# Performance work log

Measured on AMD Instinct MI355X. Metric: run time of the kernel, lower is better.

## Reference

```python
import jax, jax.numpy as jnp
import numpy as np

B, H, W, C = 64, 224, 224, 3
P = 16
DIM = 768
DEPTH = 12
NH, DH = 12, 64
FF = 3072
NPATCH = (H // P) * (W // P)   # 196
L = NPATCH + 1                 # 197 tokens (CLS + patches)
KEEP = int(L * (1.0 - 0.75))   # 49 unmasked tokens


def setup_inputs() -> dict:
    key = jax.random.key(0)
    ks = jax.random.split(key, 16)
    s = 0.02
    inp = {
        'inputs': jax.random.normal(ks[0], (B, H, W, C), jnp.float32),
        'conv_w': jax.random.normal(ks[1], (P, P, C, DIM), jnp.float32) * s,
        'ct':     jax.random.normal(ks[2], (1, 1, DIM), jnp.float32) * s,
        'pe':     jax.random.normal(ks[3], (1, L, DIM), jnp.float32) * s,
        'ln1_s': jnp.ones((DEPTH, DIM), jnp.float32),
        'ln1_b': jnp.zeros((DEPTH, DIM), jnp.float32),
        'qkv_w': jax.random.normal(ks[4], (DEPTH, DIM, 3 * NH * DH), jnp.float32) * s,
        'proj_w': jax.random.normal(ks[5], (DEPTH, NH * DH, DIM), jnp.float32) * s,
        'ln2_s': jnp.ones((DEPTH, DIM), jnp.float32),
        'ln2_b': jnp.zeros((DEPTH, DIM), jnp.float32),
        'w1': jax.random.normal(ks[6], (DEPTH, DIM, FF), jnp.float32) * s,
        'b1': jnp.zeros((DEPTH, FF), jnp.float32),
        'w2': jax.random.normal(ks[7], (DEPTH, FF, DIM), jnp.float32) * s,
        'b2': jnp.zeros((DEPTH, DIM), jnp.float32),
        # Faithful to original: permutation of arange(1, L+1); max value 197
        # is out-of-range and gets clamped by JAX gather, exactly as upstream.
        'mask_idx': jax.random.permutation(ks[8], jnp.arange(1, L + 1))[:KEEP].astype(jnp.int32),
    }
    return inp


def _layernorm(x, scale, bias, eps=1e-9):
    m = jnp.mean(x, axis=-1, keepdims=True)
    v = jnp.var(x, axis=-1, keepdims=True)
    return (x - m) * jax.lax.rsqrt(v + eps) * scale + bias


def _encoder(x, layer_params):
    # x: [B, KEEP, DIM]; layer_params leaves stacked on axis 0 (DEPTH)
    inv_sqrt_d = 1.0 / jnp.sqrt(jnp.float32(DH))

    def block(x, p):
        ln1s, ln1b, qw, pw, ln2s, ln2b, w1, b1, w2, b2 = p
        h = _layernorm(x, ln1s, ln1b)
        qkv = h @ qw                                   # [B, Lk, 3*NH*DH]
        q, k, v = jnp.split(qkv, 3, axis=-1)
        def heads(t):
            return t.reshape(x.shape[0], -1, NH, DH).transpose(0, 2, 1, 3)
        q, k, v = heads(q), heads(k), heads(v)         # [B, NH, Lk, DH]
        att = jax.nn.softmax(jnp.einsum('bhqd,bhkd->bhqk', q, k) * inv_sqrt_d)
        o = jnp.einsum('bhqk,bhkd->bhqd', att, v)
        o = o.transpose(0, 2, 1, 3).reshape(x.shape[0], -1, NH * DH) @ pw
        x = x + o
        h2 = _layernorm(x, ln2s, ln2b)
        x = x + (jax.nn.gelu(h2 @ w1 + b1) @ w2 + b2)
        return x, None

    x, _ = jax.lax.scan(block, x, layer_params)
    return x


def reference(inputs, conv_w, ct, pe, ln1_s, ln1_b, qkv_w, proj_w,
              ln2_s, ln2_b, w1, b1, w2, b2, mask_idx):
    # patch embed: stride-P conv, no bias
    out = jax.lax.conv_general_dilated(
        inputs, conv_w, window_strides=(P, P), padding='VALID',
        dimension_numbers=('NHWC', 'HWIO', 'NHWC'))      # [B, 14, 14, DIM]
    out = out.reshape(out.shape[0], -1, out.shape[3])     # [B, 196, DIM]
    out = jnp.concatenate((jnp.repeat(ct, out.shape[0], axis=0), out), axis=1)
    out = out + pe                                        # [B, 197, DIM]
    patches = out[:, mask_idx]                            # [B, 49, DIM]
    layer_params = (ln1_s, ln1_b, qkv_w, proj_w, ln2_s, ln2_b, w1, b1, w2, b2)
    return _encoder(patches, layer_params)
```

## Files before the change

### kernel.cpp

```cpp
#include <hip/hip_runtime.h>
#include <hip/hip_bf16.h>
#include <math.h>

#define DIMV   768
#define BATCH  64
#define KEEPT  49
#define MTOK   (BATCH*KEEPT)
#define NHEADS 12
#define DHEAD  64
#define FFV    3072
#define NDEPTH 12

typedef short short8 __attribute__((ext_vector_type(8)));
typedef float floatx4 __attribute__((ext_vector_type(4)));
typedef unsigned short ushort;
typedef unsigned short ushortx8 __attribute__((ext_vector_type(8)));

__device__ __forceinline__ ushort f2bf(float f) {
  __hip_bfloat16 h = __float2bfloat16(f);
  return *(ushort*)&h;
}

__device__ __forceinline__ void async_cp16(const void* g, void* l) {
  __builtin_amdgcn_global_load_lds((const __attribute__((address_space(1))) void*)g,
                                   (__attribute__((address_space(3))) void*)l,
                                   16, 0, 0);
}

__global__ __launch_bounds__(256) void gather_patches(
    const float* __restrict__ inp, const int* __restrict__ mask,
    __hip_bfloat16* __restrict__ apix)
{
  int gid = blockIdx.x * 256 + threadIdx.x;
  if (gid >= MTOK * DIMV) return;
  int r = gid / DIMV, k = gid - r * DIMV;
  int b = r / KEEPT, t = r - b * KEEPT;
  int j = mask[t];
  j = j < 0 ? 0 : (j > 196 ? 196 : j);
  float v = 0.f;
  if (j > 0) {
    int p  = j - 1, py = p / 14, px = p - py * 14;
    int ky = k / 48, rem = k - ky * 48, kx = rem / 3, c = rem - kx * 3;
    v = inp[(((b * 224) + py * 16 + ky) * 224 + px * 16 + kx) * 3 + c];
  }
  apix[gid] = __float2bfloat16(v);
}

__global__ __launch_bounds__(256) void layernorm_k(
    const float* __restrict__ x, const float* __restrict__ sc,
    const float* __restrict__ bi, __hip_bfloat16* __restrict__ out)
{
  __shared__ float red[8];
  int r = blockIdx.x;
  const float* xr = x + (size_t)r * DIMV;
  int t = threadIdx.x;
  float v[3];
  float s = 0.f, ss = 0.f;
#pragma unroll
  for (int i = 0; i < 3; i++) {
    float a = xr[t + i * 256];
    v[i] = a; s += a; ss += a * a;
  }
#pragma unroll
  for (int off = 32; off > 0; off >>= 1) {
    s  += __shfl_down(s,  off, 64);
    ss += __shfl_down(ss, off, 64);
  }
  int wave = t >> 6, lane = t & 63;
  if (lane == 0) { red[wave] = s; red[4 + wave] = ss; }
  __syncthreads();
  if (t == 0) {
    float a  = red[0] + red[1] + red[2] + red[3];
    float b2 = red[4] + red[5] + red[6] + red[7];
    float m  = a * (1.f / DIMV);
    float var = b2 * (1.f / DIMV) - m * m;
    red[0] = m;
    red[1] = rsqrtf(var + 1e-9f);
  }
  __syncthreads();
  float m = red[0], rs = red[1];
  __hip_bfloat16* outr = out + (size_t)r * DIMV;
#pragma unroll
  for (int i = 0; i < 3; i++) {
    int d = t + i * 256;
    outr[d] = __float2bfloat16((v[i] - m) * rs * sc[d] + bi[d]);
  }
}

__device__ __forceinline__ void transpose_tile64(
    const float* __restrict__ src, __hip_bfloat16* __restrict__ dst,
    int R, int C, int tr, int tcc)
{
  __shared__ float lds[64][65];
  const int tid = threadIdx.x;
  const int r0 = tr * 64, c0 = tcc * 64;
  const int lr = tid >> 4, lc4 = (tid & 15) * 4;
#pragma unroll
  for (int p = 0; p < 4; p++) {
    float4 v = *(const float4*)(src + (size_t)(r0 + p * 16 + lr) * C + c0 + lc4);
    lds[p * 16 + lr][lc4 + 0] = v.x;
    lds[p * 16 + lr][lc4 + 1] = v.y;
    lds[p * 16 + lr][lc4 + 2] = v.z;
    lds[p * 16 + lr][lc4 + 3] = v.w;
  }
  __syncthreads();
  const int c = tid >> 2, rc = (tid & 3) * 8;
  ushortx8 o0, o1;
#pragma unroll
  for (int j = 0; j < 8; j++) o0[j] = f2bf(lds[rc + j][c]);
#pragma unroll
  for (int j = 0; j < 8; j++) o1[j] = f2bf(lds[rc + 32 + j][c]);
  ushort* drow = (ushort*)dst + (size_t)(c0 + c) * R + r0;
  *(ushortx8*)(drow + rc)      = o0;
  *(ushortx8*)(drow + rc + 32) = o1;
}

__global__ __launch_bounds__(256) void transpose_one(
    const float* __restrict__ src, __hip_bfloat16* __restrict__ dst, int R, int C)
{
  int tc = C >> 6;
  transpose_tile64(src, dst, R, C, blockIdx.x / tc, blockIdx.x % tc);
}

#define QKV_TE  ((size_t)2304*768)
#define PROJ_TE ((size_t)768*768)
#define W1_TE   ((size_t)3072*768)
#define W2_TE   ((size_t)768*3072)
#define LSTRIDE (QKV_TE + PROJ_TE + W1_TE + W2_TE)
#define CW_TPG  4

struct CwTile { const float* s; ushort* d; int R, C; };

__global__ __launch_bounds__(256) void convert_weights(
    const float* __restrict__ qkv_w, const float* __restrict__ proj_w,
    const float* __restrict__ w1, const float* __restrict__ w2,
    __hip_bfloat16* __restrict__ dstBase, int layer0, size_t dstStride)
{
  __shared__ float lds[2][64][65];
  const int l = layer0 + blockIdx.y;
  __hip_bfloat16* dl = dstBase + (size_t)blockIdx.y * dstStride;
  const int tid = threadIdx.x;
  const int lr = tid >> 4, lc4 = (tid & 15) * 4;
  const int oc = tid >> 2, orc = (tid & 3) * 8;

  auto resolve = [&](int tile) -> CwTile {
    const float* src; __hip_bfloat16* dst; int R, C, t0;
    if (tile < 432)       { src = qkv_w  + (size_t)l*768*2304; dst = dl;                        R=768;  C=2304; t0=tile; }
    else if (tile < 576)  { src = proj_w + (size_t)l*768*768;  dst = dl + QKV_TE;               R=768;  C=768;  t0=tile-432; }
    else if (tile < 1152) { src = w1     + (size_t)l*768*3072; dst = dl + QKV_TE+PROJ_TE;       R=768;  C=3072; t0=tile-576; }
    else                  { src = w2     + (size_t)l*3072*768; dst = dl + QKV_TE+PROJ_TE+W1_TE; R=3072; C=768;  t0=tile-1152; }
    int tc = C >> 6, tr = t0 / tc, tcc = t0 % tc;
    CwTile r;
    r.s = src + (size_t)(tr * 64) * C + tcc * 64;
    r.d = (ushort*)dst + (size_t)(tcc * 64) * R + tr * 64;
    r.R = R; r.C = C;
    return r;
  };

  const int tbase = blockIdx.x * CW_TPG;
  CwTile cti = resolve(tbase);
  float4 rv[4];
#pragma unroll
  for (int p = 0; p < 4; p++)
    rv[p] = *(const float4*)(cti.s + (size_t)(p * 16 + lr) * cti.C + lc4);

  int cur = 0;
  for (int ti = 0; ti < CW_TPG; ti++) {
#pragma unroll
    for (int p = 0; p < 4; p++) {
      lds[cur][p * 16 + lr][lc4 + 0] = rv[p].x;
      lds[cur][p * 16 + lr][lc4 + 1] = rv[p].y;
      lds[cur][p * 16 + lr][lc4 + 2] = rv[p].z;
      lds[cur][p * 16 + lr][lc4 + 3] = rv[p].w;
    }
    __syncthreads();
    CwTile nti;
    if (ti + 1 < CW_TPG) {
      nti = resolve(tbase + ti + 1);
#pragma unroll
      for (int p = 0; p < 4; p++)
        rv[p] = *(const float4*)(nti.s + (size_t)(p * 16 + lr) * nti.C + lc4);
    }
    ushortx8 o0, o1;
#pragma unroll
    for (int j = 0; j < 8; j++) o0[j] = f2bf(lds[cur][orc + j][oc]);
#pragma unroll
    for (int j = 0; j < 8; j++) o1[j] = f2bf(lds[cur][orc + 32 + j][oc]);
    ushort* drow = cti.d + (size_t)oc * cti.R;
    *(ushortx8*)(drow + orc)      = o0;
    *(ushortx8*)(drow + orc + 32) = o1;
    if (ti + 1 < CW_TPG) cti = nti;
    cur ^= 1;
  }
}

enum { EPI_NONE = 0, EPI_RESID = 1, EPI_BIAS_GELU = 2, EPI_BIAS_RESID = 3,
       EPI_EMBED = 4 };

template <int EPI, bool OUT_BF16>
__device__ __forceinline__ void gemm_epilogue_elem(
    float u, int row, int col, int N,
    const float* __restrict__ Cin, const float* __restrict__ bias,
    const float* __restrict__ pe, const int* __restrict__ mask,
    void* __restrict__ Cout)
{
  if (EPI == EPI_BIAS_GELU || EPI == EPI_BIAS_RESID) u += bias[col];
  if (EPI == EPI_BIAS_GELU) {
    float t3 = u * u * u;
    u = 0.5f * u * (1.f + tanhf(0.7978845608028654f * (u + 0.044715f * t3)));
  }
  if (EPI == EPI_RESID || EPI == EPI_BIAS_RESID) u += Cin[(size_t)row * N + col];
  if (EPI == EPI_EMBED) {
    int t = row % KEEPT;
    int j = mask[t];
    j = j < 0 ? 0 : (j > 196 ? 196 : j);
    if (j == 0) u = bias[col];
    u += pe[(size_t)j * DIMV + col];
  }
  if (OUT_BF16)
    ((__hip_bfloat16*)Cout)[(size_t)row * N + col] = __float2bfloat16(u);
  else
    ((float*)Cout)[(size_t)row * N + col] = u;
}

template <int EPI, bool OUT_BF16>
__global__ __launch_bounds__(256) void gemm_mfma(
    const ushort* __restrict__ A, const ushort* __restrict__ Bt,
    const float* __restrict__ Cin, const float* __restrict__ bias,
    const float* __restrict__ pe, const int* __restrict__ mask,
    void* __restrict__ Cout, int M, int N, int K)
{
  __shared__ ushort As[2][128 * 64];
  __shared__ ushort Bs[2][64 * 64];

  const int tid  = threadIdx.x;
  const int wave = tid >> 6, lane = tid & 63;
  const int bm = blockIdx.y, bn = blockIdx.x;
  const int fr = lane & 15, fc = lane >> 4;

  floatx4 acc[2][4];
#pragma unroll
  for (int i = 0; i < 2; i++)
#pragma unroll
    for (int j = 0; j < 4; j++) { floatx4 z = {0.f,0.f,0.f,0.f}; acc[i][j] = z; }

  const int lrow   = lane >> 3;
  const int lchunk = ((lane & 7) ^ lrow) * 8;
  const ushort* aSrc[4];
#pragma unroll
  for (int i = 0; i < 4; i++) {
    int row = bm * 128 + wave * 32 + i * 8 + lrow;
    row = row < M - 1 ? row : M - 1;
    aSrc[i] = A + (size_t)row * K + lchunk;
  }
  const ushort* bSrc[2];
#pragma unroll
  for (int i = 0; i < 2; i++) {
    int row = bn * 64 + wave * 16 + i * 8 + lrow;
    bSrc[i] = Bt + (size_t)row * K + lchunk;
  }

  const int NT = K >> 6;
  {
    ushort* aD = &As[0][(wave * 32) * 64];
#pragma unroll
    for (int i = 0; i < 4; i++) async_cp16(aSrc[i], aD + i * 8 * 64);
    ushort* bD = &Bs[0][(wave * 16) * 64];
#pragma unroll
    for (int i = 0; i < 2; i++) async_cp16(bSrc[i], bD + i * 8 * 64);
  }
  asm volatile("s_waitcnt vmcnt(0)" ::: "memory");
  __builtin_amdgcn_s_barrier();
  __builtin_amdgcn_sched_barrier(0);

  int cur = 0;
  for (int t = 0; t < NT; t++) {
    if (t + 1 < NT) {
      const int k0 = (t + 1) << 6;
      ushort* aD = &As[cur ^ 1][(wave * 32) * 64];
#pragma unroll
      for (int i = 0; i < 4; i++) async_cp16(aSrc[i] + k0, aD + i * 8 * 64);
      ushort* bD = &Bs[cur ^ 1][(wave * 16) * 64];
#pragma unroll
      for (int i = 0; i < 2; i++) async_cp16(bSrc[i] + k0, bD + i * 8 * 64);
    }

    const ushort* Ab = As[cur];
    const ushort* Bb = Bs[cur];
    short8 af[2][2], bf[2][4];
#pragma unroll
    for (int kk = 0; kk < 2; kk++) {
      const int cbase = kk * 4 + fc;
      const int slot  = (cbase ^ (fr & 7)) * 8;
#pragma unroll
      for (int mt = 0; mt < 2; mt++)
        af[kk][mt] = *(const short8*)&Ab[(wave * 32 + mt * 16 + fr) * 64 + slot];
#pragma unroll
      for (int nt = 0; nt < 4; nt++)
        bf[kk][nt] = *(const short8*)&Bb[(nt * 16 + fr) * 64 + slot];
    }
    __builtin_amdgcn_s_setprio(1);
#pragma unroll
    for (int kk = 0; kk < 2; kk++)
#pragma unroll
      for (int mt = 0; mt < 2; mt++)
#pragma unroll
        for (int nt = 0; nt < 4; nt++)
          acc[mt][nt] = __builtin_amdgcn_mfma_f32_16x16x32_bf16(
              af[kk][mt], bf[kk][nt], acc[mt][nt], 0, 0, 0);
    __builtin_amdgcn_s_setprio(0);

    if (t + 1 < NT) {
      asm volatile("s_waitcnt vmcnt(0)" ::: "memory");
      __builtin_amdgcn_s_barrier();
      __builtin_amdgcn_sched_barrier(0);
    }
    cur ^= 1;
  }

  const int colb = bn * 64 + fr;
  const int rq   = fc * 4;
#pragma unroll
  for (int mt = 0; mt < 2; mt++)
#pragma unroll
    for (int r = 0; r < 4; r++) {
      int row = bm * 128 + wave * 32 + mt * 16 + rq + r;
      if (row >= M) continue;
#pragma unroll
      for (int nt = 0; nt < 4; nt++)
        gemm_epilogue_elem<EPI, OUT_BF16>(acc[mt][nt][r], row, colb + nt * 16,
                                          N, Cin, bias, pe, mask, Cout);
    }
}

template <int EPI, bool OUT_BF16>
__global__ __launch_bounds__(512) void gemm_big(
    const ushort* __restrict__ A, const ushort* __restrict__ Bt,
    const float* __restrict__ Cin, const float* __restrict__ bias,
    const float* __restrict__ pe, const int* __restrict__ mask,
    void* __restrict__ Cout, int M, int N, int K)
{
  __shared__ ushort As[2][128 * 64];
  __shared__ ushort Bs[2][128 * 64];

  const int tid  = threadIdx.x;
  const int wave = tid >> 6, lane = tid & 63;
  const int bm = blockIdx.y, bn = blockIdx.x;
  const int fr = lane & 15, fc = lane >> 4;
  const int wm0 = (wave >> 2) * 64, wn0 = (wave & 3) * 32;

  floatx4 acc[4][2];
#pragma unroll
  for (int i = 0; i < 4; i++)
#pragma unroll
    for (int j = 0; j < 2; j++) { floatx4 z = {0.f,0.f,0.f,0.f}; acc[i][j] = z; }

  const int lrow   = lane >> 3;
  const int lchunk = ((lane & 7) ^ lrow) * 8;
  const ushort* aSrc[2];
#pragma unroll
  for (int i = 0; i < 2; i++) {
    int row = bm * 128 + wave * 16 + i * 8 + lrow;
    row = row < M - 1 ? row : M - 1;
    aSrc[i] = A + (size_t)row * K + lchunk;
  }
  const ushort* bSrc[2];
#pragma unroll
  for (int i = 0; i < 2; i++) {
    int row = bn * 128 + wave * 16 + i * 8 + lrow;
    bSrc[i] = Bt + (size_t)row * K + lchunk;
  }

  const int NT = K >> 6;
  {
    ushort* aD = &As[0][(wave * 16) * 64];
#pragma unroll
    for (int i = 0; i < 2; i++) async_cp16(aSrc[i], aD + i * 8 * 64);
    ushort* bD = &Bs[0][(wave * 16) * 64];
#pragma unroll
    for (int i = 0; i < 2; i++) async_cp16(bSrc[i], bD + i * 8 * 64);
  }
  asm volatile("s_waitcnt vmcnt(0)" ::: "memory");
  __builtin_amdgcn_s_barrier();
  __builtin_amdgcn_sched_barrier(0);

  int cur = 0;
  for (int t = 0; t < NT; t++) {
    if (t + 1 < NT) {
      const int k0 = (t + 1) << 6;
      ushort* aD = &As[cur ^ 1][(wave * 16) * 64];
#pragma unroll
      for (int i = 0; i < 2; i++) async_cp16(aSrc[i] + k0, aD + i * 8 * 64);
      ushort* bD = &Bs[cur ^ 1][(wave * 16) * 64];
#pragma unroll
      for (int i = 0; i < 2; i++) async_cp16(bSrc[i] + k0, bD + i * 8 * 64);
    }

    const ushort* Ab = As[cur];
    const ushort* Bb = Bs[cur];
    short8 af[2][4], bf[2][2];
#pragma unroll
    for (int kk = 0; kk < 2; kk++) {
      const int cbase = kk * 4 + fc;
      const int slot  = (cbase ^ (fr & 7)) * 8;
#pragma unroll
      for (int mt = 0; mt < 4; mt++)
        af[kk][mt] = *(const short8*)&Ab[(wm0 + mt * 16 + fr) * 64 + slot];
#pragma unroll
      for (int nt = 0; nt < 2; nt++)
        bf[kk][nt] = *(const short8*)&Bb[(wn0 + nt * 16 + fr) * 64 + slot];
    }
    __builtin_amdgcn_s_setprio(1);
#pragma unroll
    for (int kk = 0; kk < 2; kk++)
#pragma unroll
      for (int mt = 0; mt < 4; mt++)
#pragma unroll
        for (int nt = 0; nt < 2; nt++)
          acc[mt][nt] = __builtin_amdgcn_mfma_f32_16x16x32_bf16(
              af[kk][mt], bf[kk][nt], acc[mt][nt], 0, 0, 0);
    __builtin_amdgcn_s_setprio(0);

    if (t + 1 < NT) {
      asm volatile("s_waitcnt vmcnt(0)" ::: "memory");
      __builtin_amdgcn_s_barrier();
      __builtin_amdgcn_sched_barrier(0);
    }
    cur ^= 1;
  }

  const int colb = bn * 128 + wn0 + fr;
  const int rq   = fc * 4;
#pragma unroll
  for (int mt = 0; mt < 4; mt++)
#pragma unroll
    for (int r = 0; r < 4; r++) {
      int row = bm * 128 + wm0 + mt * 16 + rq + r;
      if (row >= M) continue;
#pragma unroll
      for (int nt = 0; nt < 2; nt++)
        gemm_epilogue_elem<EPI, OUT_BF16>(acc[mt][nt][r], row, colb + nt * 16,
                                          N, Cin, bias, pe, mask, Cout);
    }
}

__global__ __launch_bounds__(256) void attn_mfma(
    const ushort* __restrict__ qkv, ushort* __restrict__ o)
{
  __shared__ ushort qA[64 * 72];
  __shared__ ushort kB[64 * 72];
  __shared__ ushort vT[64 * 72];
  __shared__ ushort pA[64 * 72];
  const int b = blockIdx.x, hh = blockIdx.y;
  const int tid = threadIdx.x;
  const int wave = tid >> 6, lane = tid & 63;
  const int fr = lane & 15, fc = lane >> 4;

  const ushort* base = qkv + (size_t)b * KEEPT * (3 * DIMV) + hh * 64;

#pragma unroll
  for (int it = 0; it < 2; it++) {
    int r  = it * 32 + wave * 8 + (lane >> 3);
    int cc = (lane & 7) * 8;
    short8 qv = {0,0,0,0,0,0,0,0};
    short8 kv = {0,0,0,0,0,0,0,0};
    if (r < KEEPT) {
      const ushort* row = base + (size_t)r * (3 * DIMV);
      qv = *(const short8*)(row + cc);
      kv = *(const short8*)(row + DIMV + cc);
    }
    *(short8*)&qA[r * 72 + cc] = qv;
    *(short8*)&kB[r * 72 + cc] = kv;
  }
  for (int r = wave; r < 64; r += 4) {
    ushort v = 0;
    if (r < KEEPT) v = base[(size_t)r * (3 * DIMV) + 2 * DIMV + lane];
    vT[lane * 72 + r] = v;
  }
  __syncthreads();

  const int q0 = wave * 16;
  floatx4 sacc[4];
#pragma unroll
  for (int nt = 0; nt < 4; nt++) { floatx4 z = {0.f,0.f,0.f,0.f}; sacc[nt] = z; }

#pragma unroll
  for (int kk = 0; kk < 2; kk++) {
    const int ch = kk * 32 + fc * 8;
    short8 af = *(const short8*)&qA[(q0 + fr) * 72 + ch];
#pragma unroll
    for (int nt = 0; nt < 4; nt++) {
      short8 bf = *(const short8*)&kB[(nt * 16 + fr) * 72 + ch];
      sacc[nt] = __builtin_amdgcn_mfma_f32_16x16x32_bf16(af, bf, sacc[nt], 0, 0, 0);
    }
  }

  float inv[4];
#pragma unroll
  for (int r = 0; r < 4; r++) {
    float mx = -1e30f;
#pragma unroll
    for (int nt = 0; nt < 4; nt++) {
      float s = sacc[nt][r] * 0.125f;
      if (nt == 3 && fr >= 1) s = -1e30f;
      sacc[nt][r] = s;
      mx = fmaxf(mx, s);
    }
    mx = fmaxf(mx, __shfl_xor(mx, 1, 64));
    mx = fmaxf(mx, __shfl_xor(mx, 2, 64));
    mx = fmaxf(mx, __shfl_xor(mx, 4, 64));
    mx = fmaxf(mx, __shfl_xor(mx, 8, 64));
    float sum = 0.f;
#pragma unroll
    for (int nt = 0; nt < 4; nt++) {
      float e = __expf(sacc[nt][r] - mx);
      sacc[nt][r] = e;
      sum += e;
    }
    sum += __shfl_xor(sum, 1, 64);
    sum += __shfl_xor(sum, 2, 64);
    sum += __shfl_xor(sum, 4, 64);
    sum += __shfl_xor(sum, 8, 64);
    inv[r] = 1.f / sum;
  }

#pragma unroll
  for (int r = 0; r < 4; r++)
#pragma unroll
    for (int nt = 0; nt < 4; nt++)
      pA[(q0 + fc * 4 + r) * 72 + nt * 16 + fr] = f2bf(sacc[nt][r]);
  __syncthreads();

  floatx4 oacc[4];
#pragma unroll
  for (int nt = 0; nt < 4; nt++) { floatx4 z = {0.f,0.f,0.f,0.f}; oacc[nt] = z; }

#pragma unroll
  for (int kk = 0; kk < 2; kk++) {
    const int ch = kk * 32 + fc * 8;
    short8 af = *(const short8*)&pA[(q0 + fr) * 72 + ch];
#pragma unroll
    for (int nt = 0; nt < 4; nt++) {
      short8 bf = *(const short8*)&vT[(nt * 16 + fr) * 72 + ch];
      oacc[nt] = __builtin_amdgcn_mfma_f32_16x16x32_bf16(af, bf, oacc[nt], 0, 0, 0);
    }
  }

  ushort* obase = o + (size_t)b * KEEPT * DIMV + hh * 64;
#pragma unroll
  for (int r = 0; r < 4; r++) {
    int q = q0 + fc * 4 + r;
    if (q < KEEPT) {
#pragma unroll
      for (int nt = 0; nt < 4; nt++)
        obase[(size_t)q * DIMV + nt * 16 + fr] = f2bf(oacc[nt][r] * inv[r]);
    }
  }
}

extern "C" void kernel_launch(void* const* d_in, const int* in_sizes, int n_in,
                              void* d_out, int out_size, void* d_ws, size_t ws_size,
                              hipStream_t stream)
{
  (void)in_sizes; (void)n_in; (void)out_size;
  const float* inputs = (const float*)d_in[0];
  const float* conv_w = (const float*)d_in[1];
  const float* ct     = (const float*)d_in[2];
  const float* pe     = (const float*)d_in[3];
  const float* ln1_s  = (const float*)d_in[4];
  const float* ln1_b  = (const float*)d_in[5];
  const float* qkv_w  = (const float*)d_in[6];
  const float* proj_w = (const float*)d_in[7];
  const float* ln2_s  = (const float*)d_in[8];
  const float* ln2_b  = (const float*)d_in[9];
  const float* w1     = (const float*)d_in[10];
  const float* b1     = (const float*)d_in[11];
  const float* w2     = (const float*)d_in[12];
  const float* b2     = (const float*)d_in[13];
  const int*   mask   = (const int*)d_in[14];
  float* out = (float*)d_out;

  char* wsb = (char*)d_ws;
  float*          x     = (float*)wsb;
  __hip_bfloat16* h     = (__hip_bfloat16*)(wsb + 9633792);
  __hip_bfloat16* big   = (__hip_bfloat16*)(wsb + 9633792 + 4816896);
  __hip_bfloat16* convT = (__hip_bfloat16*)(wsb + 9633792 + 4816896 + 19267584);
  __hip_bfloat16* wbuf  = (__hip_bfloat16*)(wsb + 9633792 + 4816896 + 19267584 + 1179648);
  const size_t base_bytes = 9633792ull + 4816896 + 19267584 + 1179648;
  const bool all_mode = ws_size >= base_bytes + 12ull * LSTRIDE * 2;

  __hip_bfloat16* apix = h;
  __hip_bfloat16* qkv  = big;
  __hip_bfloat16* g    = big;

  dim3 blk(256);
  dim3 blk2(512);
  const int nelem = MTOK * DIMV;
  const int nblk  = (nelem + 255) / 256;
  const int mg    = (MTOK + 127) / 128;

  transpose_one<<<144, blk, 0, stream>>>(conv_w, convT, 768, 768);
  if (all_mode)
    convert_weights<<<dim3(1728 / CW_TPG, 12), blk, 0, stream>>>(
        qkv_w, proj_w, w1, w2, wbuf, 0, LSTRIDE);

  gather_patches<<<nblk, blk, 0, stream>>>(inputs, mask, apix);
  gemm_mfma<EPI_EMBED, false><<<dim3(12, mg), blk, 0, stream>>>(
      (const ushort*)apix, (const ushort*)convT, nullptr, ct, pe, mask, x,
      MTOK, DIMV, DIMV);

  for (int l = 0; l < NDEPTH; l++) {
    __hip_bfloat16* wl = wbuf + (all_mode ? (size_t)l * LSTRIDE : 0);
    if (!all_mode)
      convert_weights<<<dim3(1728 / CW_TPG, 1), blk, 0, stream>>>(
          qkv_w, proj_w, w1, w2, wbuf, l, 0);
    const ushort* qkvT  = (const ushort*)wl;
    const ushort* projT = (const ushort*)(wl + QKV_TE);
    const ushort* w1T   = (const ushort*)(wl + QKV_TE + PROJ_TE);
    const ushort* w2T   = (const ushort*)(wl + QKV_TE + PROJ_TE + W1_TE);

    layernorm_k<<<MTOK, blk, 0, stream>>>(x, ln1_s + l * DIMV, ln1_b + l * DIMV, h);
    gemm_big<EPI_NONE, true><<<dim3(18, mg), blk2, 0, stream>>>(
        (const ushort*)h, qkvT, nullptr, nullptr, nullptr, nullptr, qkv,
        MTOK, 3 * DIMV, DIMV);
    attn_mfma<<<dim3(BATCH, NHEADS), blk, 0, stream>>>(
        (const ushort*)qkv, (ushort*)h);
    gemm_mfma<EPI_RESID, false><<<dim3(12, mg), blk, 0, stream>>>(
        (const ushort*)h, projT, x, nullptr, nullptr, nullptr, x,
        MTOK, DIMV, DIMV);
    layernorm_k<<<MTOK, blk, 0, stream>>>(x, ln2_s + l * DIMV, ln2_b + l * DIMV, h);
    gemm_big<EPI_BIAS_GELU, true><<<dim3(24, mg), blk2, 0, stream>>>(
        (const ushort*)h, w1T, nullptr, b1 + (size_t)l * FFV, nullptr, nullptr, g,
        MTOK, FFV, DIMV);
    float* dst = (l == NDEPTH - 1) ? out : x;
    gemm_mfma<EPI_BIAS_RESID, false><<<dim3(12, mg), blk, 0, stream>>>(
        (const ushort*)g, w2T, x, b2 + (size_t)l * DIMV, nullptr, nullptr, dst,
        MTOK, DIMV, FFV);
  }
}
```

Before: 2.251 ms.

## Triple-buffer GEMM shared-memory tiles with two-stage async prefetch

Both MFMA GEMM kernels move from double to triple buffering of the A/B tiles in LDS. They prefetch two K-tiles ahead and use a partial vmcnt wait, so one tile's loads can stay in flight across the barrier. This aims to hide global-load latency that the old vmcnt(0) wait at the end of every iteration exposed. In exchange, LDS use grows by half (96KB for gemm_big), which may lower occupancy. The wait counts must exactly match the number of async copies issued per stage.

```diff
diff --git a/kernel.cpp b/kernel.cpp
--- a/kernel.cpp
+++ b/kernel.cpp
@@ -230,8 +230,8 @@
     const float* __restrict__ pe, const int* __restrict__ mask,
     void* __restrict__ Cout, int M, int N, int K)
 {
-  __shared__ ushort As[2][128 * 64];
-  __shared__ ushort Bs[2][64 * 64];
+  __shared__ ushort As[3][128 * 64];
+  __shared__ ushort Bs[3][64 * 64];
 
   const int tid  = threadIdx.x;
   const int wave = tid >> 6, lane = tid & 63;
@@ -261,26 +261,32 @@
   }
 
   const int NT = K >> 6;
-  {
-    ushort* aD = &As[0][(wave * 32) * 64];
-#pragma unroll
-    for (int i = 0; i < 4; i++) async_cp16(aSrc[i], aD + i * 8 * 64);
-    ushort* bD = &Bs[0][(wave * 16) * 64];
-#pragma unroll
-    for (int i = 0; i < 2; i++) async_cp16(bSrc[i], bD + i * 8 * 64);
-  }
-  asm volatile("s_waitcnt vmcnt(0)" ::: "memory");
-  __builtin_amdgcn_s_barrier();
-  __builtin_amdgcn_sched_barrier(0);
+
+#pragma unroll
+  for (int pb = 0; pb < 2; pb++) {
+    const int k0 = pb << 6;
+    ushort* aD = &As[pb][(wave * 32) * 64];
+#pragma unroll
+    for (int i = 0; i < 4; i++) async_cp16(aSrc[i] + k0, aD + i * 8 * 64);
+    ushort* bD = &Bs[pb][(wave * 16) * 64];
+#pragma unroll
+    for (int i = 0; i < 2; i++) async_cp16(bSrc[i] + k0, bD + i * 8 * 64);
+  }
 
   int cur = 0;
   for (int t = 0; t < NT; t++) {
-    if (t + 1 < NT) {
-      const int k0 = (t + 1) << 6;
-      ushort* aD = &As[cur ^ 1][(wave * 32) * 64];
+    if (t + 1 < NT) asm volatile("s_waitcnt vmcnt(6)" ::: "memory");
+    else            asm volatile("s_waitcnt vmcnt(0)" ::: "memory");
+    __builtin_amdgcn_s_barrier();
+    __builtin_amdgcn_sched_barrier(0);
+
+    if (t + 2 < NT) {
+      const int sb = cur >= 1 ? cur - 1 : 2;
+      const int k0 = (t + 2) << 6;
+      ushort* aD = &As[sb][(wave * 32) * 64];
 #pragma unroll
       for (int i = 0; i < 4; i++) async_cp16(aSrc[i] + k0, aD + i * 8 * 64);
-      ushort* bD = &Bs[cur ^ 1][(wave * 16) * 64];
+      ushort* bD = &Bs[sb][(wave * 16) * 64];
 #pragma unroll
       for (int i = 0; i < 2; i++) async_cp16(bSrc[i] + k0, bD + i * 8 * 64);
     }
@@ -310,12 +316,7 @@
               af[kk][mt], bf[kk][nt], acc[mt][nt], 0, 0, 0);
     __builtin_amdgcn_s_setprio(0);
 
-    if (t + 1 < NT) {
-      asm volatile("s_waitcnt vmcnt(0)" ::: "memory");
-      __builtin_amdgcn_s_barrier();
-      __builtin_amdgcn_sched_barrier(0);
-    }
-    cur ^= 1;
+    cur = cur + 1 == 3 ? 0 : cur + 1;
   }
 
   const int colb = bn * 64 + fr;
@@ -340,8 +341,8 @@
     const float* __restrict__ pe, const int* __restrict__ mask,
     void* __restrict__ Cout, int M, int N, int K)
 {
-  __shared__ ushort As[2][128 * 64];
-  __shared__ ushort Bs[2][128 * 64];
+  __shared__ ushort As[3][128 * 64];
+  __shared__ ushort Bs[3][128 * 64];
 
   const int tid  = threadIdx.x;
   const int wave = tid >> 6, lane = tid & 63;
@@ -372,26 +373,32 @@
   }
 
   const int NT = K >> 6;
-  {
-    ushort* aD = &As[0][(wave * 16) * 64];
-#pragma unroll
-    for (int i = 0; i < 2; i++) async_cp16(aSrc[i], aD + i * 8 * 64);
-    ushort* bD = &Bs[0][(wave * 16) * 64];
-#pragma unroll
-    for (int i = 0; i < 2; i++) async_cp16(bSrc[i], bD + i * 8 * 64);
-  }
-  asm volatile("s_waitcnt vmcnt(0)" ::: "memory");
-  __builtin_amdgcn_s_barrier();
-  __builtin_amdgcn_sched_barrier(0);
+
+#pragma unroll
+  for (int pb = 0; pb < 2; pb++) {
+    const int k0 = pb << 6;
+    ushort* aD = &As[pb][(wave * 16) * 64];
+#pragma unroll
+    for (int i = 0; i < 2; i++) async_cp16(aSrc[i] + k0, aD + i * 8 * 64);
+    ushort* bD = &Bs[pb][(wave * 16) * 64];
+#pragma unroll
+    for (int i = 0; i < 2; i++) async_cp16(bSrc[i] + k0, bD + i * 8 * 64);
+  }
 
   int cur = 0;
   for (int t = 0; t < NT; t++) {
-    if (t + 1 < NT) {
-      const int k0 = (t + 1) << 6;
-      ushort* aD = &As[cur ^ 1][(wave * 16) * 64];
+    if (t + 1 < NT) asm volatile("s_waitcnt vmcnt(4)" ::: "memory");
+    else            asm volatile("s_waitcnt vmcnt(0)" ::: "memory");
+    __builtin_amdgcn_s_barrier();
+    __builtin_amdgcn_sched_barrier(0);
+
+    if (t + 2 < NT) {
+      const int sb = cur >= 1 ? cur - 1 : 2;
+      const int k0 = (t + 2) << 6;
+      ushort* aD = &As[sb][(wave * 16) * 64];
 #pragma unroll
       for (int i = 0; i < 2; i++) async_cp16(aSrc[i] + k0, aD + i * 8 * 64);
-      ushort* bD = &Bs[cur ^ 1][(wave * 16) * 64];
+      ushort* bD = &Bs[sb][(wave * 16) * 64];
 #pragma unroll
       for (int i = 0; i < 2; i++) async_cp16(bSrc[i] + k0, bD + i * 8 * 64);
     }
@@ -421,12 +428,7 @@
               af[kk][mt], bf[kk][nt], acc[mt][nt], 0, 0, 0);
     __builtin_amdgcn_s_setprio(0);
 
-    if (t + 1 < NT) {
-      asm volatile("s_waitcnt vmcnt(0)" ::: "memory");
-      __builtin_amdgcn_s_barrier();
-      __builtin_amdgcn_sched_barrier(0);
-    }
-    cur ^= 1;
+    cur = cur + 1 == 3 ? 0 : cur + 1;
   }
 
   const int colb = bn * 128 + wn0 + fr;
```

New measurement: 2.527 ms. 12.3% more time.
